# Kernel tuning notes

Measured on AMD Instinct MI355X. Metric: run time of the kernel, lower is better.

The kernel has to match this reference:

```python
import jax, jax.numpy as jnp
import numpy as np

N_DELTA, N_THETA, N_GAMMA = 64, 128, 512
N_TOTAL = N_DELTA + N_THETA + N_GAMMA  # 704
N_CLASSES = 1000
N_STEPS = 5
DT = 0.01
COUPLING = 2.0      # coupling_strength
PAC_DT = 0.3        # delta->theta phase-amplitude coupling depth
PAC_TG = 0.3        # theta->gamma phase-amplitude coupling depth
SPARSITY = 0.1      # PhaseToRateConverter sparsity (fraction of active units)
SHARP = 10.0        # softness of the 'soft' sparsification gate
TWO_PI = 2.0 * np.pi
B = 65536


def setup_inputs() -> dict:
    key = jax.random.key(0)
    k1, k2, k3, k4 = jax.random.split(key, 4)
    x = jax.random.normal(k1, (B, N_TOTAL), dtype=jnp.float32)
    # per-sample random initial phases in [0,1), scaled to [0,2pi) inside reference
    phase0 = jax.random.uniform(k2, (B, N_TOTAL), dtype=jnp.float32)
    W = jax.random.normal(k3, (N_CLASSES, N_TOTAL), dtype=jnp.float32) * 0.02
    b = jax.random.normal(k4, (N_CLASSES,), dtype=jnp.float32) * 0.02
    return {"x": x, "phase0": phase0, "W": W, "b": b}


def _kuramoto(phi):
    # mean-field within-band Kuramoto coupling: K * mean_j sin(phi_j - phi_i)
    S = jnp.mean(jnp.sin(phi), axis=-1, keepdims=True)
    C = jnp.mean(jnp.cos(phi), axis=-1, keepdims=True)
    return COUPLING * (S * jnp.cos(phi) - C * jnp.sin(phi))


def _mean_phase(phi):
    # circular mean phase of a band, shape (B,1)
    return jnp.arctan2(jnp.mean(jnp.sin(phi), axis=-1, keepdims=True),
                       jnp.mean(jnp.cos(phi), axis=-1, keepdims=True))


def _forward(x, phase0, W, b):
    freqs = jnp.concatenate([
        jnp.linspace(1.0, 4.0, N_DELTA),    # delta band Hz
        jnp.linspace(4.0, 8.0, N_THETA),    # theta band Hz
        jnp.linspace(30.0, 80.0, N_GAMMA),  # gamma band Hz
    ]).astype(x.dtype)
    phi = phase0 * TWO_PI                       # (B, N_TOTAL)
    amp = 1.0 + jnp.abs(x) * 0.01               # amplitude seeded by |x|*0.01 on unit base
    d = slice(0, N_DELTA)
    t = slice(N_DELTA, N_DELTA + N_THETA)
    g = slice(N_DELTA + N_THETA, N_TOTAL)

    def step(carry, _):
        phi, amp = carry
        dphi = TWO_PI * freqs + jnp.concatenate(
            [_kuramoto(phi[:, d]), _kuramoto(phi[:, t]), _kuramoto(phi[:, g])], axis=-1)
        psi_d = _mean_phase(phi[:, d])
        psi_t = _mean_phase(phi[:, t])
        # PAC: theta amplitude driven by delta phase, gamma amplitude by theta phase
        damp = jnp.concatenate([
            jnp.zeros_like(amp[:, d]),
            PAC_DT * amp[:, t] * jnp.cos(psi_d),
            PAC_TG * amp[:, g] * jnp.cos(psi_t),
        ], axis=-1)
        phi_new = jnp.mod(phi + DT * dphi, TWO_PI)
        amp_new = amp + DT * damp
        return (phi_new, amp_new), None

    (phi, amp), _ = jax.lax.scan(step, (phi, amp), None, length=N_STEPS)

    # PhaseToRateConverter, mode='soft': raw rate then soft top-(sparsity) gate
    raw = amp * 0.5 * (1.0 + jnp.cos(phi))                              # (B, N_TOTAL)
    thr = jnp.quantile(raw, 1.0 - SPARSITY, axis=-1, keepdims=True)    # per-sample threshold
    rate = raw * jax.nn.sigmoid((raw - thr) * SHARP)
    return rate @ W.T + b                                               # (B, N_CLASSES)


def reference(x, phase0, W, b):
    return _forward(x, phase0, W, b)
```

## Files before the change

### kernel.cpp

```cpp
#include <hip/hip_runtime.h>

#define NB 65536
#define NTOT 704
#define NCLS 1000
#define NPAD 1024
#define KDIM 704

typedef __attribute__((ext_vector_type(8))) short bf16x8;
typedef __attribute__((ext_vector_type(4))) float f32x4;
typedef __attribute__((ext_vector_type(2))) float f32x2;

#define WB_ELEMS (NPAD * KDIM)
#define LUT_DC_OFF (2u * (WB_ELEMS + 46137344u))
#define LUT_DS_OFF (LUT_DC_OFF + NTOT * 4u)

__device__ __forceinline__ f32x2 sp(float x) { return (f32x2){x, x}; }

template <int CTRL>
__device__ __forceinline__ float dpp_shuf(float v) {
  return __int_as_float(__builtin_amdgcn_update_dpp(0, __float_as_int(v), CTRL, 0xF, 0xF, true));
}
__device__ __forceinline__ float swz16(float v) {
  return __int_as_float(__builtin_amdgcn_ds_swizzle(__float_as_int(v), 0x401F));
}
__device__ __forceinline__ float wsum_f(float v) {
  v += dpp_shuf<0xB1>(v);
  v += dpp_shuf<0x4E>(v);
  v += dpp_shuf<0x141>(v);
  v += dpp_shuf<0x140>(v);
  v += swz16(v);
  v += __shfl_xor(v, 32, 64);
  return v;
}
__device__ __forceinline__ float wmax_f(float v) {
  v = fmaxf(v, dpp_shuf<0xB1>(v));
  v = fmaxf(v, dpp_shuf<0x4E>(v));
  v = fmaxf(v, dpp_shuf<0x141>(v));
  v = fmaxf(v, dpp_shuf<0x140>(v));
  v = fmaxf(v, swz16(v));
  v = fmaxf(v, __shfl_xor(v, 32, 64));
  return v;
}
__device__ __forceinline__ float wmin_f(float v) {
  v = fminf(v, dpp_shuf<0xB1>(v));
  v = fminf(v, dpp_shuf<0x4E>(v));
  v = fminf(v, dpp_shuf<0x141>(v));
  v = fminf(v, dpp_shuf<0x140>(v));
  v = fminf(v, swz16(v));
  v = fminf(v, __shfl_xor(v, 32, 64));
  return v;
}

__device__ __forceinline__ unsigned short f2bf(float v) {
  unsigned u = __float_as_uint(v);
  u = (u + 0x7FFFu + ((u >> 16) & 1u)) >> 16;
  return (unsigned short)u;
}

__global__ __launch_bounds__(256) void convw_kernel(const float* __restrict__ W,
                                                    unsigned short* __restrict__ Wb,
                                                    float* __restrict__ dcL,
                                                    float* __restrict__ dsL) {
  int i = blockIdx.x * 256 + threadIdx.x;
  if (i < NTOT) {
    float f;
    if (i < 64)       f = 1.0f + 3.0f * (float)i * (1.0f / 63.0f);
    else if (i < 192) f = 4.0f + 4.0f * (float)(i - 64) * (1.0f / 127.0f);
    else              f = 30.0f + 50.0f * (float)(i - 192) * (1.0f / 511.0f);
    const float rev = 0.01f * f;
    dcL[i] = __builtin_amdgcn_cosf(rev);
    dsL[i] = __builtin_amdgcn_sinf(rev);
  }
  if (i >= NPAD * KDIM) return;
  int n = i / KDIM;
  float v = (n < NCLS) ? W[i] : 0.0f;
  Wb[i] = f2bf(v);
}

__global__ __launch_bounds__(256) void sim_kernel(const float* __restrict__ x,
                                                  const float* __restrict__ p0,
                                                  const float* __restrict__ dcL,
                                                  const float* __restrict__ dsL,
                                                  unsigned short* __restrict__ rateb) {
  const int wave = threadIdx.x >> 6;
  const int lane = threadIdx.x & 63;
  const int sample = blockIdx.x * 4 + wave;
  const size_t base = (size_t)sample * NTOT;

  float sD, cD, ampD, dcD, dsD;
  f32x2 sPp[5], cPp[5], dc2[5], ds2[5], amp2[5];
  {
    const float p = p0[base + lane];
    sD = __builtin_amdgcn_sinf(p);
    cD = __builtin_amdgcn_cosf(p);
    ampD = fmaf(fabsf(x[base + lane]), 0.01f, 1.0f);
    dcD = dcL[lane]; dsD = dsL[lane];
  }
#pragma unroll
  for (int pr = 0; pr < 5; ++pr) {
    const int i0 = (1 + 2 * pr) * 64 + lane;
    const int i1 = i0 + 64;
    const float pa = p0[base + i0], pb = p0[base + i1];
    sPp[pr] = (f32x2){__builtin_amdgcn_sinf(pa), __builtin_amdgcn_sinf(pb)};
    cPp[pr] = (f32x2){__builtin_amdgcn_cosf(pa), __builtin_amdgcn_cosf(pb)};
    amp2[pr] = (f32x2){fmaf(fabsf(x[base + i0]), 0.01f, 1.0f),
                       fmaf(fabsf(x[base + i1]), 0.01f, 1.0f)};
    dc2[pr] = (f32x2){dcL[i0], dcL[i1]};
    ds2[pr] = (f32x2){dsL[i0], dsL[i1]};
  }

  float prodT = 1.0f, prodG = 1.0f;

#pragma unroll
  for (int st = 0; st < 5; ++st) {
    const float Sd = wsum_f(sD);
    const float Cd = wsum_f(cD);
    const float St = wsum_f(sPp[0].x + sPp[0].y);
    const float Ct = wsum_f(cPp[0].x + cPp[0].y);
    const f32x2 gs = (sPp[1] + sPp[2]) + (sPp[3] + sPp[4]);
    const f32x2 gc = (cPp[1] + cPp[2]) + (cPp[3] + cPp[4]);
    const float Sg = wsum_f(gs.x + gs.y);
    const float Cg = wsum_f(gc.x + gc.y);
    const float cpd = Cd * __builtin_amdgcn_rsqf(fmaf(Sd, Sd, Cd * Cd));
    const float cpt = Ct * __builtin_amdgcn_rsqf(fmaf(St, St, Ct * Ct));
    prodT *= fmaf(0.003f, cpd, 1.0f);
    prodG *= fmaf(0.003f, cpt, 1.0f);
    const float sdm = Sd * (0.02f / 64.0f),  cdm = Cd * (0.02f / 64.0f);
    const float stm = St * (0.02f / 128.0f), ctm = Ct * (0.02f / 128.0f);
    const float sgm = Sg * (0.02f / 512.0f), cgm = Cg * (0.02f / 512.0f);
    {
      const float eps = fmaf(-cdm, sD, sdm * cD);
      const float e2 = eps * eps;
      const float ce = fmaf(-0.5f, e2, 1.0f);
      const float cd_ = fmaf(-dsD, eps, dcD * ce);
      const float sd_ = fmaf(dcD, eps, dsD * ce);
      const float sn = fmaf(cD, sd_, sD * cd_);
      const float cn = fmaf(-sD, sd_, cD * cd_);
      sD = sn; cD = cn;
    }
#pragma unroll
    for (int pr = 0; pr < 5; ++pr) {
      const f32x2 Sm = sp(pr == 0 ? stm : sgm);
      const f32x2 Cm = sp(pr == 0 ? ctm : cgm);
      const f32x2 s2 = sPp[pr], c2 = cPp[pr];
      const f32x2 eps = Sm * c2 - Cm * s2;
      const f32x2 e2 = eps * eps;
      const f32x2 ce = sp(1.0f) - sp(0.5f) * e2;
      const f32x2 cosd = dc2[pr] * ce - ds2[pr] * eps;
      const f32x2 sind = ds2[pr] * ce + dc2[pr] * eps;
      sPp[pr] = s2 * cosd + c2 * sind;
      cPp[pr] = c2 * cosd - s2 * sind;
    }
  }

  float raw[11];
  unsigned kk[11];
  {
    const float h = 0.5f * ampD;
    raw[0] = fmaf(h, cD, h);
  }
  const float hT = 0.5f * prodT, hG = 0.5f * prodG;
#pragma unroll
  for (int pr = 0; pr < 5; ++pr) {
    const f32x2 h2 = amp2[pr] * sp(pr == 0 ? hT : hG);
    const f32x2 r2 = h2 * cPp[pr] + h2;
    raw[1 + 2 * pr] = r2.x;
    raw[2 + 2 * pr] = r2.y;
  }
#pragma unroll
  for (int e = 0; e < 11; ++e) kk[e] = (unsigned)(raw[e] * 8192.0f);

  unsigned pre = 0;
#pragma unroll
  for (int bit = 13; bit >= 0; --bit) {
    const unsigned u = pre | ((1u << bit) - 1u);
    int cnt = 0;
#pragma unroll
    for (int e = 0; e < 11; ++e) cnt += (int)__popcll(__ballot(kk[e] <= u));
    if (cnt < 633) pre |= (1u << bit);
  }

  int clt = 0, ceq = 0;
#pragma unroll
  for (int e = 0; e < 11; ++e) {
    clt += (int)__popcll(__ballot(kk[e] < pre));
    ceq += (int)__popcll(__ballot(kk[e] == pre));
  }

  const float qv = 0.9f * 703.0f;
  float thr;
  if (clt + ceq >= 634) {
    thr = ((float)pre + 0.5f) * (1.0f / 8192.0f);
  } else {
    float mx = -1.0f, mn = 3.0e38f;
#pragma unroll
    for (int e = 0; e < 11; ++e) {
      mx = fmaxf(mx, (kk[e] == pre) ? raw[e] : -1.0f);
      mn = fminf(mn, (kk[e] > pre) ? raw[e] : 3.0e38f);
    }
    const float S632 = wmax_f(mx);
    const float S633 = wmin_f(mn);
    thr = S632 * (633.0f - qv) + S633 * (qv - 632.0f);
  }

#pragma unroll
  for (int e = 0; e < 11; ++e) {
    const float r = raw[e];
    const float t = __expf((thr - r) * 10.0f);
    const float sg = __builtin_amdgcn_rcpf(1.0f + t);
    rateb[base + e * 64 + lane] = f2bf(r * sg);
  }
}

#define BM 128
#define BN 128
#define BK 64

__device__ __forceinline__ void gload16(const unsigned short* g, unsigned short* l) {
  __builtin_amdgcn_global_load_lds((const __attribute__((address_space(1))) void*)g,
                                   (__attribute__((address_space(3))) void*)l,
                                   16, 0, 0);
}

__global__ __launch_bounds__(256) void gemm_kernel(const unsigned short* __restrict__ A,
                                                   const unsigned short* __restrict__ Bw,
                                                   const float* __restrict__ bias,
                                                   float* __restrict__ C) {
  __shared__ unsigned short lA[BM * BK];
  __shared__ unsigned short lB[BN * BK];
  const int tid  = threadIdx.x;
  const int wave = tid >> 6;
  const int lane = tid & 63;

  const int bid = blockIdx.x;
  const int swz = (bid & 7) * 512 + (bid >> 3);
  const int bm = swz >> 3;
  const int bn = swz & 7;

  const int wr = wave >> 1;
  const int wc = wave & 1;

  f32x4 acc[4][4];
#pragma unroll
  for (int i = 0; i < 4; ++i)
#pragma unroll
    for (int j = 0; j < 4; ++j) acc[i][j] = (f32x4){0.f, 0.f, 0.f, 0.f};

  const int lrow = lane >> 3;
  const int lk   = (lane & 7) * 8;

  for (int kt = 0; kt < KDIM / BK; ++kt) {
    const int k0 = kt * BK;
#pragma unroll
    for (int i = 0; i < 4; ++i) {
      const int c = wave * 4 + i;
      const size_t garow = (size_t)(bm * BM + c * 8 + lrow);
      gload16(A + garow * KDIM + k0 + lk, lA + c * 512);
      const size_t gbrow = (size_t)(bn * BN + c * 8 + lrow);
      gload16(Bw + gbrow * KDIM + k0 + lk, lB + c * 512);
    }
    __syncthreads();
#pragma unroll
    for (int ks = 0; ks < 2; ++ks) {
      bf16x8 av[4], bv[4];
#pragma unroll
      for (int m = 0; m < 4; ++m)
        av[m] = *(const bf16x8*)&lA[(wr * 64 + m * 16 + (lane & 15)) * BK + ks * 32 + (lane >> 4) * 8];
#pragma unroll
      for (int n = 0; n < 4; ++n)
        bv[n] = *(const bf16x8*)&lB[(wc * 64 + n * 16 + (lane & 15)) * BK + ks * 32 + (lane >> 4) * 8];
#pragma unroll
      for (int m = 0; m < 4; ++m)
#pragma unroll
        for (int n = 0; n < 4; ++n)
          acc[m][n] = __builtin_amdgcn_mfma_f32_16x16x32_bf16(av[m], bv[n], acc[m][n], 0, 0, 0);
    }
    __syncthreads();
  }

  const int crow0 = bm * BM + wr * 64;
  const int ccol0 = bn * BN + wc * 64;
  const int rql = (lane >> 4) * 4;
  const int cl  = lane & 15;
#pragma unroll
  for (int n = 0; n < 4; ++n) {
    const int col = ccol0 + n * 16 + cl;
    if (col < NCLS) {
      const float bb = bias[col];
#pragma unroll
      for (int m = 0; m < 4; ++m) {
#pragma unroll
        for (int r = 0; r < 4; ++r) {
          const int row = crow0 + m * 16 + rql + r;
          C[(size_t)row * NCLS + col] = acc[m][n][r] + bb;
        }
      }
    }
  }
}

extern "C" void kernel_launch(void* const* d_in, const int* in_sizes, int n_in,
                              void* d_out, int out_size, void* d_ws, size_t ws_size,
                              hipStream_t stream) {
  const float* x    = (const float*)d_in[0];
  const float* p0   = (const float*)d_in[1];
  const float* W    = (const float*)d_in[2];
  const float* bias = (const float*)d_in[3];
  float* out = (float*)d_out;

  unsigned short* Wb    = (unsigned short*)d_ws;
  unsigned short* rateb = (unsigned short*)d_ws + WB_ELEMS;
  float* dcL = (float*)((char*)d_ws + LUT_DC_OFF);
  float* dsL = (float*)((char*)d_ws + LUT_DS_OFF);

  convw_kernel<<<dim3((NPAD * KDIM + 255) / 256), dim3(256), 0, stream>>>(W, Wb, dcL, dsL);
  sim_kernel<<<dim3(NB / 4), dim3(256), 0, stream>>>(x, p0, dcL, dsL, rateb);
  gemm_kernel<<<dim3((NB / BM) * (NPAD / BN)), dim3(256), 0, stream>>>(rateb, Wb, bias, out);
}
```

Baseline: 359.9 us.

## Double-buffer GEMM LDS tiles and XOR-swizzle k-blocks to avoid bank conflicts

Allocates two LDS buffers for the A and B tiles and issues the next k-tile's global-to-LDS loads before computing on the current one, so load latency can overlap with MFMA work. It also XOR-swizzles the 16-byte k-block position by row on store and read, to reduce LDS bank conflicts on the fragment reads. Doubling LDS to 64KB per block may reduce the number of resident blocks per CU.

New measurement: 362.4 us. Within noise of the previous version (+0.7%).

```diff
diff --git a/kernel.cpp b/kernel.cpp
--- a/kernel.cpp
+++ b/kernel.cpp
@@ -215,6 +215,7 @@
 #define BM 128
 #define BN 128
 #define BK 64
+#define NKT (KDIM / BK)
 
 __device__ __forceinline__ void gload16(const unsigned short* g, unsigned short* l) {
   __builtin_amdgcn_global_load_lds((const __attribute__((address_space(1))) void*)g,
@@ -226,8 +227,8 @@
                                                    const unsigned short* __restrict__ Bw,
                                                    const float* __restrict__ bias,
                                                    float* __restrict__ C) {
-  __shared__ unsigned short lA[BM * BK];
-  __shared__ unsigned short lB[BN * BK];
+  __shared__ unsigned short lA[2][BM * BK];
+  __shared__ unsigned short lB[2][BN * BK];
   const int tid  = threadIdx.x;
   const int wave = tid >> 6;
   const int lane = tid & 63;
@@ -246,29 +247,45 @@
 #pragma unroll
     for (int j = 0; j < 4; ++j) acc[i][j] = (f32x4){0.f, 0.f, 0.f, 0.f};
 
-  const int lrow = lane >> 3;
-  const int lk   = (lane & 7) * 8;
-
-  for (int kt = 0; kt < KDIM / BK; ++kt) {
-    const int k0 = kt * BK;
-#pragma unroll
-    for (int i = 0; i < 4; ++i) {
-      const int c = wave * 4 + i;
-      const size_t garow = (size_t)(bm * BM + c * 8 + lrow);
-      gload16(A + garow * KDIM + k0 + lk, lA + c * 512);
-      const size_t gbrow = (size_t)(bn * BN + c * 8 + lrow);
-      gload16(Bw + gbrow * KDIM + k0 + lk, lB + c * 512);
-    }
-    __syncthreads();
+  const int lrow  = lane >> 3;
+  const int lkblk = (((lane & 7) ^ lrow)) * 8;
+
+  const unsigned short* Abase = A  + (size_t)(bm * BM) * KDIM;
+  const unsigned short* Bbase = Bw + (size_t)(bn * BN) * KDIM;
+
+#define STAGE(buf, kt)                                                          \
+  {                                                                             \
+    const int k0_ = (kt) * BK;                                                  \
+    _Pragma("unroll")                                                           \
+    for (int i_ = 0; i_ < 4; ++i_) {                                            \
+      const int c_ = wave * 4 + i_;                                             \
+      gload16(Abase + (size_t)(c_ * 8 + lrow) * KDIM + k0_ + lkblk,             \
+              &lA[buf][c_ * 512]);                                              \
+      gload16(Bbase + (size_t)(c_ * 8 + lrow) * KDIM + k0_ + lkblk,             \
+              &lB[buf][c_ * 512]);                                              \
+    }                                                                           \
+  }
+
+  STAGE(0, 0);
+  __syncthreads();
+
+  int buf = 0;
+  for (int kt = 0; kt < NKT; ++kt) {
+    if (kt < NKT - 1) STAGE(buf ^ 1, kt + 1);
 #pragma unroll
     for (int ks = 0; ks < 2; ++ks) {
       bf16x8 av[4], bv[4];
-#pragma unroll
-      for (int m = 0; m < 4; ++m)
-        av[m] = *(const bf16x8*)&lA[(wr * 64 + m * 16 + (lane & 15)) * BK + ks * 32 + (lane >> 4) * 8];
-#pragma unroll
-      for (int n = 0; n < 4; ++n)
-        bv[n] = *(const bf16x8*)&lB[(wc * 64 + n * 16 + (lane & 15)) * BK + ks * 32 + (lane >> 4) * 8];
+      const int slot = 8 * ((((ks << 2) | (lane >> 4)) ^ (lane & 7)));
+#pragma unroll
+      for (int m = 0; m < 4; ++m) {
+        const int r = wr * 64 + m * 16 + (lane & 15);
+        av[m] = *(const bf16x8*)&lA[buf][r * BK + slot];
+      }
+#pragma unroll
+      for (int n = 0; n < 4; ++n) {
+        const int r = wc * 64 + n * 16 + (lane & 15);
+        bv[n] = *(const bf16x8*)&lB[buf][r * BK + slot];
+      }
 #pragma unroll
       for (int m = 0; m < 4; ++m)
 #pragma unroll
@@ -276,6 +293,7 @@
           acc[m][n] = __builtin_amdgcn_mfma_f32_16x16x32_bf16(av[m], bv[n], acc[m][n], 0, 0, 0);
     }
     __syncthreads();
+    buf ^= 1;
   }
 
   const int crow0 = bm * BM + wr * 64;
```

## Rework GEMM into 256x256 tiles with triple-buffered async LDS pipeline and swizzle

Applied to the files above, without the earlier changes.

The GEMM moves from 128x128 tiles with a single LDS buffer to 256x256 tiles with 512 threads, three LDS stages filled by direct global-to-LDS loads, explicit vmcnt waits, an XOR bank swizzle and raised MFMA priority. The aim is to overlap loads with MFMA work, cut LDS bank conflicts and raise operand reuse per tile. Separately, the phase-rotation update in the simulation kernel drops the second-order eps^2 term of the small-angle cosine, saving a few FLOPs per step. That slightly changes numerics, and the larger tile raises register and LDS pressure, which lowers occupancy.

Result: faster. 331.3 us (-7.9%).

```diff
diff --git a/kernel.cpp b/kernel.cpp
--- a/kernel.cpp
+++ b/kernel.cpp
@@ -130,10 +130,8 @@
     const float sgm = Sg * (0.02f / 512.0f), cgm = Cg * (0.02f / 512.0f);
     {
       const float eps = fmaf(-cdm, sD, sdm * cD);
-      const float e2 = eps * eps;
-      const float ce = fmaf(-0.5f, e2, 1.0f);
-      const float cd_ = fmaf(-dsD, eps, dcD * ce);
-      const float sd_ = fmaf(dcD, eps, dsD * ce);
+      const float cd_ = fmaf(-dsD, eps, dcD);
+      const float sd_ = fmaf(dcD, eps, dsD);
       const float sn = fmaf(cD, sd_, sD * cd_);
       const float cn = fmaf(-sD, sd_, cD * cd_);
       sD = sn; cD = cn;
@@ -144,10 +142,8 @@
       const f32x2 Cm = sp(pr == 0 ? ctm : cgm);
       const f32x2 s2 = sPp[pr], c2 = cPp[pr];
       const f32x2 eps = Sm * c2 - Cm * s2;
-      const f32x2 e2 = eps * eps;
-      const f32x2 ce = sp(1.0f) - sp(0.5f) * e2;
-      const f32x2 cosd = dc2[pr] * ce - ds2[pr] * eps;
-      const f32x2 sind = ds2[pr] * ce + dc2[pr] * eps;
+      const f32x2 cosd = dc2[pr] - ds2[pr] * eps;
+      const f32x2 sind = ds2[pr] + dc2[pr] * eps;
       sPp[pr] = s2 * cosd + c2 * sind;
       cPp[pr] = c2 * cosd - s2 * sind;
     }
@@ -212,9 +208,10 @@
   }
 }
 
-#define BM 128
-#define BN 128
-#define BK 64
+#define BM2 256
+#define BN2 256
+#define BK2 32
+#define NK2 (KDIM / BK2)
 
 __device__ __forceinline__ void gload16(const unsigned short* g, unsigned short* l) {
   __builtin_amdgcn_global_load_lds((const __attribute__((address_space(1))) void*)g,
@@ -222,64 +219,93 @@
                                    16, 0, 0);
 }
 
-__global__ __launch_bounds__(256) void gemm_kernel(const unsigned short* __restrict__ A,
+__global__ __launch_bounds__(512) void gemm_kernel(const unsigned short* __restrict__ A,
                                                    const unsigned short* __restrict__ Bw,
                                                    const float* __restrict__ bias,
                                                    float* __restrict__ C) {
-  __shared__ unsigned short lA[BM * BK];
-  __shared__ unsigned short lB[BN * BK];
+  __shared__ __align__(16) unsigned short lsA[3 * BM2 * BK2];
+  __shared__ __align__(16) unsigned short lsB[3 * BN2 * BK2];
   const int tid  = threadIdx.x;
   const int wave = tid >> 6;
   const int lane = tid & 63;
 
   const int bid = blockIdx.x;
-  const int swz = (bid & 7) * 512 + (bid >> 3);
-  const int bm = swz >> 3;
-  const int bn = swz & 7;
-
-  const int wr = wave >> 1;
-  const int wc = wave & 1;
-
-  f32x4 acc[4][4];
-#pragma unroll
-  for (int i = 0; i < 4; ++i)
+  const int swz = (bid & 7) * 128 + (bid >> 3);
+  const int bm = swz >> 2;
+  const int bn = swz & 3;
+
+  const int wr = wave >> 2;
+  const int wc = wave & 3;
+
+  f32x4 acc[8][4];
+#pragma unroll
+  for (int i = 0; i < 8; ++i)
 #pragma unroll
     for (int j = 0; j < 4; ++j) acc[i][j] = (f32x4){0.f, 0.f, 0.f, 0.f};
 
-  const int lrow = lane >> 3;
-  const int lk   = (lane & 7) * 8;
-
-  for (int kt = 0; kt < KDIM / BK; ++kt) {
-    const int k0 = kt * BK;
-#pragma unroll
-    for (int i = 0; i < 4; ++i) {
-      const int c = wave * 4 + i;
-      const size_t garow = (size_t)(bm * BM + c * 8 + lrow);
-      gload16(A + garow * KDIM + k0 + lk, lA + c * 512);
-      const size_t gbrow = (size_t)(bn * BN + c * 8 + lrow);
-      gload16(Bw + gbrow * KDIM + k0 + lk, lB + c * 512);
-    }
-    __syncthreads();
-#pragma unroll
-    for (int ks = 0; ks < 2; ++ks) {
-      bf16x8 av[4], bv[4];
-#pragma unroll
-      for (int m = 0; m < 4; ++m)
-        av[m] = *(const bf16x8*)&lA[(wr * 64 + m * 16 + (lane & 15)) * BK + ks * 32 + (lane >> 4) * 8];
+  const int rowi = tid >> 2;
+  const int ksrc = (tid & 3) ^ ((tid >> 3) & 3);
+
+  const unsigned short* Abase = A  + (size_t)(bm * BM2) * KDIM;
+  const unsigned short* Bbase = Bw + (size_t)(bn * BN2) * KDIM;
+
+#define STAGE2(buf, kt)                                                        \
+  {                                                                            \
+    const int k0_ = (kt) * BK2;                                                \
+    _Pragma("unroll")                                                          \
+    for (int g_ = 0; g_ < 2; ++g_) {                                           \
+      gload16(Abase + (size_t)(g_ * 128 + rowi) * KDIM + k0_ + ksrc * 8,       \
+              lsA + (buf) * (BM2 * BK2) + g_ * 4096 + tid * 8);                \
+      gload16(Bbase + (size_t)(g_ * 128 + rowi) * KDIM + k0_ + ksrc * 8,       \
+              lsB + (buf) * (BN2 * BK2) + g_ * 4096 + tid * 8);                \
+    }                                                                          \
+  }
+
+  STAGE2(0, 0);
+  STAGE2(1, 1);
+
+  const int l15 = lane & 15;
+  const int kq  = lane >> 4;
+
+  int cur = 0;
+#pragma unroll 1
+  for (int t = 0; t < NK2; ++t) {
+    int sb = cur + 2; if (sb >= 3) sb -= 3;
+    if (t < NK2 - 2) STAGE2(sb, t + 2);
+    if (t < NK2 - 2)      asm volatile("s_waitcnt vmcnt(8)" ::: "memory");
+    else if (t == NK2 - 2) asm volatile("s_waitcnt vmcnt(4)" ::: "memory");
+    else                   asm volatile("s_waitcnt vmcnt(0)" ::: "memory");
+    asm volatile("s_barrier" ::: "memory");
+
+    bf16x8 af[8], bf[4];
+    const unsigned short* la = lsA + cur * (BM2 * BK2);
+    const unsigned short* lb = lsB + cur * (BN2 * BK2);
+#pragma unroll
+    for (int m = 0; m < 8; ++m) {
+      const int row = wr * 128 + m * 16 + l15;
+      const int slot = kq ^ ((row >> 1) & 3);
+      af[m] = *(const bf16x8*)&la[row * BK2 + slot * 8];
+    }
+#pragma unroll
+    for (int n = 0; n < 4; ++n) {
+      const int row = wc * 64 + n * 16 + l15;
+      const int slot = kq ^ ((row >> 1) & 3);
+      bf[n] = *(const bf16x8*)&lb[row * BK2 + slot * 8];
+    }
+    asm volatile("s_waitcnt lgkmcnt(0)" ::: "memory");
+    __builtin_amdgcn_s_setprio(1);
+#pragma unroll
+    for (int m = 0; m < 8; ++m)
 #pragma unroll
       for (int n = 0; n < 4; ++n)
-        bv[n] = *(const bf16x8*)&lB[(wc * 64 + n * 16 + (lane & 15)) * BK + ks * 32 + (lane >> 4) * 8];
-#pragma unroll
-      for (int m = 0; m < 4; ++m)
-#pragma unroll
-        for (int n = 0; n < 4; ++n)
-          acc[m][n] = __builtin_amdgcn_mfma_f32_16x16x32_bf16(av[m], bv[n], acc[m][n], 0, 0, 0);
-    }
-    __syncthreads();
-  }
-
-  const int crow0 = bm * BM + wr * 64;
-  const int ccol0 = bn * BN + wc * 64;
+        acc[m][n] = __builtin_amdgcn_mfma_f32_16x16x32_bf16(af[m], bf[n], acc[m][n], 0, 0, 0);
+    __builtin_amdgcn_s_setprio(0);
+    asm volatile("s_barrier" ::: "memory");
+    cur += 1; if (cur >= 3) cur -= 3;
+  }
+
+  const int crow0 = bm * BM2 + wr * 128;
+  const int ccol0 = bn * BN2 + wc * 64;
   const int rql = (lane >> 4) * 4;
   const int cl  = lane & 15;
 #pragma unroll
@@ -288,7 +314,7 @@
     if (col < NCLS) {
       const float bb = bias[col];
 #pragma unroll
-      for (int m = 0; m < 4; ++m) {
+      for (int m = 0; m < 8; ++m) {
 #pragma unroll
         for (int r = 0; r < 4; ++r) {
           const int row = crow0 + m * 16 + rql + r;
@@ -315,5 +341,5 @@
 
   convw_kernel<<<dim3((NPAD * KDIM + 255) / 256), dim3(256), 0, stream>>>(W, Wb, dcL, dsL);
   sim_kernel<<<dim3(NB / 4), dim3(256), 0, stream>>>(x, p0, dcL, dsL, rateb);
-  gemm_kernel<<<dim3((NB / BM) * (NPAD / BN)), dim3(256), 0, stream>>>(rateb, Wb, bias, out);
-}
+  gemm_kernel<<<dim3((NB / BM2) * (NPAD / BN2)), dim3(512), 0, stream>>>(rateb, Wb, bias, out);
+}
```

## Double-buffer A tile in LDS, read B directly from global, drop eps² term

Applied to the files above, without the earlier changes.

The GEMM now double-buffers only the activation tile in LDS, using an XOR swizzle to avoid bank conflicts, and prefetches the next k-tile while the MFMAs run. Weight fragments are loaded straight from global memory into registers, relying on cache hits because W is shared by all row blocks. Explicit waitcnt, sched barriers and setprio control the overlap. Separately, the sim kernel drops the second-order eps² correction in the small-angle rotation update, which saves a few FLOPs at some accuracy risk.

Result: slower. 368.7 us (+2.4%).

```diff
diff --git a/kernel.cpp b/kernel.cpp
--- a/kernel.cpp
+++ b/kernel.cpp
@@ -7,6 +7,7 @@
 #define KDIM 704
 
 typedef __attribute__((ext_vector_type(8))) short bf16x8;
+typedef __attribute__((ext_vector_type(4))) int i32x4;
 typedef __attribute__((ext_vector_type(4))) float f32x4;
 typedef __attribute__((ext_vector_type(2))) float f32x2;
 
@@ -130,10 +131,8 @@
     const float sgm = Sg * (0.02f / 512.0f), cgm = Cg * (0.02f / 512.0f);
     {
       const float eps = fmaf(-cdm, sD, sdm * cD);
-      const float e2 = eps * eps;
-      const float ce = fmaf(-0.5f, e2, 1.0f);
-      const float cd_ = fmaf(-dsD, eps, dcD * ce);
-      const float sd_ = fmaf(dcD, eps, dsD * ce);
+      const float cd_ = fmaf(-dsD, eps, dcD);
+      const float sd_ = fmaf(dcD, eps, dsD);
       const float sn = fmaf(cD, sd_, sD * cd_);
       const float cn = fmaf(-sD, sd_, cD * cd_);
       sD = sn; cD = cn;
@@ -144,10 +143,8 @@
       const f32x2 Cm = sp(pr == 0 ? ctm : cgm);
       const f32x2 s2 = sPp[pr], c2 = cPp[pr];
       const f32x2 eps = Sm * c2 - Cm * s2;
-      const f32x2 e2 = eps * eps;
-      const f32x2 ce = sp(1.0f) - sp(0.5f) * e2;
-      const f32x2 cosd = dc2[pr] * ce - ds2[pr] * eps;
-      const f32x2 sind = ds2[pr] * ce + dc2[pr] * eps;
+      const f32x2 cosd = dc2[pr] - ds2[pr] * eps;
+      const f32x2 sind = ds2[pr] + dc2[pr] * eps;
       sPp[pr] = s2 * cosd + c2 * sind;
       cPp[pr] = c2 * cosd - s2 * sind;
     }
@@ -212,9 +209,13 @@
   }
 }
 
-#define BM 128
-#define BN 128
-#define BK 64
+#define BK3 64
+#define NK3 (KDIM / BK3)
+
+#define FENCE __builtin_amdgcn_sched_barrier(0)
+#define BAR   do { FENCE; __builtin_amdgcn_s_barrier(); FENCE; } while (0)
+#define WVM0  do { asm volatile("s_waitcnt vmcnt(0)"); FENCE; } while (0)
+#define WLG0  do { asm volatile("s_waitcnt lgkmcnt(0)"); FENCE; } while (0)
 
 __device__ __forceinline__ void gload16(const unsigned short* g, unsigned short* l) {
   __builtin_amdgcn_global_load_lds((const __attribute__((address_space(1))) void*)g,
@@ -222,12 +223,19 @@
                                    16, 0, 0);
 }
 
-__global__ __launch_bounds__(256) void gemm_kernel(const unsigned short* __restrict__ A,
-                                                   const unsigned short* __restrict__ Bw,
-                                                   const float* __restrict__ bias,
-                                                   float* __restrict__ C) {
-  __shared__ unsigned short lA[BM * BK];
-  __shared__ unsigned short lB[BN * BK];
+__device__ __forceinline__ bf16x8 ds_read16(const unsigned short* p) {
+  i32x4 r;
+  const unsigned addr =
+      (unsigned)(unsigned long long)(const __attribute__((address_space(3))) unsigned short*)p;
+  asm volatile("ds_read_b128 %0, %1" : "=v"(r) : "v"(addr));
+  return *(bf16x8*)&r;
+}
+
+__global__ __launch_bounds__(256, 3) void gemm_kernel(const unsigned short* __restrict__ A,
+                                                      const unsigned short* __restrict__ Bw,
+                                                      const float* __restrict__ bias,
+                                                      float* __restrict__ C) {
+  __shared__ __align__(16) unsigned short lsA[2 * 8192];
   const int tid  = threadIdx.x;
   const int wave = tid >> 6;
   const int lane = tid & 63;
@@ -246,45 +254,72 @@
 #pragma unroll
     for (int j = 0; j < 4; ++j) acc[i][j] = (f32x4){0.f, 0.f, 0.f, 0.f};
 
-  const int lrow = lane >> 3;
-  const int lk   = (lane & 7) * 8;
-
-  for (int kt = 0; kt < KDIM / BK; ++kt) {
-    const int k0 = kt * BK;
-#pragma unroll
-    for (int i = 0; i < 4; ++i) {
-      const int c = wave * 4 + i;
-      const size_t garow = (size_t)(bm * BM + c * 8 + lrow);
-      gload16(A + garow * KDIM + k0 + lk, lA + c * 512);
-      const size_t gbrow = (size_t)(bn * BN + c * 8 + lrow);
-      gload16(Bw + gbrow * KDIM + k0 + lk, lB + c * 512);
-    }
-    __syncthreads();
-#pragma unroll
-    for (int ks = 0; ks < 2; ++ks) {
-      bf16x8 av[4], bv[4];
+  const int srow8 = tid >> 3;
+  const unsigned short* Ab = A + (size_t)(bm * 128) * KDIM;
+  const int l15 = lane & 15;
+  const int kq  = lane >> 4;
+
+#define SA(buf, k0)                                                                     \
+  {                                                                                     \
+    _Pragma("unroll")                                                                   \
+    for (int g_ = 0; g_ < 4; ++g_) {                                                    \
+      const int row_ = g_ * 32 + srow8;                                                 \
+      gload16(Ab + (size_t)row_ * KDIM + (k0) + ((tid & 7) ^ (row_ & 7)) * 8,           \
+              lsA + (buf) * 8192 + g_ * 2048 + tid * 8);                                \
+    }                                                                                   \
+  }
+
+  const unsigned short* bp[4];
+#pragma unroll
+  for (int n = 0; n < 4; ++n)
+    bp[n] = Bw + (size_t)(bn * 128 + wc * 64 + n * 16 + l15) * KDIM + kq * 8;
+
+  SA(0, 0)
+  FENCE;
+
+  bf16x8 af[4][2], bg[4][2];
+
+#pragma unroll 1
+  for (int t = 0; t < NK3; ++t) {
+    const int c = t & 1;
+    const unsigned short* hbuf = lsA + c * 8192;
+
+    WVM0;
+    BAR;
+#pragma unroll
+    for (int m = 0; m < 4; ++m) {
+      const int lr = wr * 64 + m * 16 + l15;
+      af[m][0] = ds_read16(&hbuf[lr * 64 + ((kq ^ (lr & 7)) * 8)]);
+      af[m][1] = ds_read16(&hbuf[lr * 64 + (((kq + 4) ^ (lr & 7)) * 8)]);
+    }
+#pragma unroll
+    for (int n = 0; n < 4; ++n) {
+      bg[n][0] = *(const bf16x8*)(bp[n]);
+      bg[n][1] = *(const bf16x8*)(bp[n] + 32);
+      bp[n] += 64;
+    }
+    if (t < NK3 - 1) { SA(c ^ 1, (t + 1) * BK3) }
+    FENCE;
+    WLG0;
+    __builtin_amdgcn_s_setprio(1);
+#pragma unroll
+    for (int kh = 0; kh < 2; ++kh)
 #pragma unroll
       for (int m = 0; m < 4; ++m)
-        av[m] = *(const bf16x8*)&lA[(wr * 64 + m * 16 + (lane & 15)) * BK + ks * 32 + (lane >> 4) * 8];
-#pragma unroll
-      for (int n = 0; n < 4; ++n)
-        bv[n] = *(const bf16x8*)&lB[(wc * 64 + n * 16 + (lane & 15)) * BK + ks * 32 + (lane >> 4) * 8];
-#pragma unroll
-      for (int m = 0; m < 4; ++m)
 #pragma unroll
         for (int n = 0; n < 4; ++n)
-          acc[m][n] = __builtin_amdgcn_mfma_f32_16x16x32_bf16(av[m], bv[n], acc[m][n], 0, 0, 0);
-    }
-    __syncthreads();
-  }
-
-  const int crow0 = bm * BM + wr * 64;
-  const int ccol0 = bn * BN + wc * 64;
+          acc[m][n] = __builtin_amdgcn_mfma_f32_16x16x32_bf16(af[m][kh], bg[n][kh],
+                                                              acc[m][n], 0, 0, 0);
+    __builtin_amdgcn_s_setprio(0);
+    FENCE;
+  }
+
+  const int crow0 = bm * 128 + wr * 64;
+  const int ccol0 = bn * 128 + wc * 64;
   const int rql = (lane >> 4) * 4;
-  const int cl  = lane & 15;
 #pragma unroll
   for (int n = 0; n < 4; ++n) {
-    const int col = ccol0 + n * 16 + cl;
+    const int col = ccol0 + n * 16 + l15;
     if (col < NCLS) {
       const float bb = bias[col];
 #pragma unroll
@@ -315,5 +350,5 @@
 
   convw_kernel<<<dim3((NPAD * KDIM + 255) / 256), dim3(256), 0, stream>>>(W, Wb, dcL, dsL);
   sim_kernel<<<dim3(NB / 4), dim3(256), 0, stream>>>(x, p0, dcL, dsL, rateb);
-  gemm_kernel<<<dim3((NB / BM) * (NPAD / BN)), dim3(256), 0, stream>>>(rateb, Wb, bias, out);
-}
+  gemm_kernel<<<dim3((NB / 128) * (NPAD / 128)), dim3(256), 0, stream>>>(rateb, Wb, bias, out);
+}
```
